# Kernel tuning notes

Measured on AMD Instinct MI355X. Metric: run time of the kernel, lower is better.

## Reference

```python
import jax, jax.numpy as jnp
import numpy as np

N_NODES = 10000
N_EDGES = 160000
MUL0 = 128   # multiplicity of 0e in node input/output
MUL1 = 64    # multiplicity of 1o in node input/output
FC_IN = 8    # radial basis size (edge_scalar_attr dim)
FC_H = 64    # fc_neurons = [64, 64]
NUM_NEIGHBORS = 16.0
ANGLE = np.pi / 8.0
MID0 = MUL0 + MUL1   # 192 scalars in irreps_mid (simplified)
MID1 = MUL0 + MUL1   # 192 vectors (1o) in irreps_mid


def _inv_sqrt(d):
    return 1.0 / np.sqrt(d)


def setup_inputs() -> dict:
    key = jax.random.key(0)
    ks = jax.random.split(key, 18)
    rn = lambda k, shape: jax.random.normal(k, shape, dtype=jnp.float32)
    inp = {
        'node_input': rn(ks[0], (N_NODES, MUL0 + 3 * MUL1)),
        'edge_attr': rn(ks[1], (N_EDGES, 4)),            # 1x0e + 1x1o spherical harmonics
        'edge_scalar_attr': rn(ks[2], (N_EDGES, FC_IN)),
        # first Linear: node_input -> (node_features || node_self_out)
        'Wa0': rn(ks[3], (MUL0, MUL0)),   # 0e -> 0e (message branch)
        'Wa1': rn(ks[4], (MUL1, MUL1)),   # 1o -> 1o (message branch)
        'Wb0': rn(ks[5], (MUL0, MUL0)),   # 0e -> 0e (self branch)
        'Wb1': rn(ks[6], (MUL1, MUL1)),   # 1o -> 1o (self branch)
        # radial MLP
        'M1': rn(ks[7], (FC_IN, FC_H)),
        'M2': rn(ks[8], (FC_H, FC_H)),
        # per-instruction TP weight generators: [FC_H, mul] ('uvu', v=1 squeezed)
        'Wtp0': rn(ks[9], (FC_H, MUL0)),   # 0e x 0e -> 0e
        'Wtp1': rn(ks[10], (FC_H, MUL0)),  # 0e x 1o -> 1o
        'Wtp2': rn(ks[11], (FC_H, MUL1)),  # 1o x 0e -> 1o
        'Wtp3': rn(ks[12], (FC_H, MUL1)),  # 1o x 1o -> 0e
        # output Linear: irreps_mid (192x0e + 192x1o) -> 128x0e + 64x1o
        'Wo0': rn(ks[13], (MID0, MUL0)),
        'Wo1': rn(ks[14], (MID1, MUL1)),
        'edge_src': jax.random.randint(ks[15], (N_EDGES,), 0, N_NODES),
        'edge_dst': jax.random.randint(ks[16], (N_EDGES,), 0, N_NODES),
    }
    return inp


def _forward(node_input, edge_attr, edge_scalar_attr,
             Wa0, Wa1, Wb0, Wb1, M1, M2,
             Wtp0, Wtp1, Wtp2, Wtp3, Wo0, Wo1,
             edge_src, edge_dst):
    n = node_input.shape[0]
    x0 = node_input[:, :MUL0]                         # [N,128] 0e
    x1 = node_input[:, MUL0:].reshape(n, MUL1, 3)     # [N,64,3] 1o

    # Linear(node_input.irreps + irreps_node_output): split into message / self
    feat0 = (x0 @ Wa0) * _inv_sqrt(MUL0)
    feat1 = jnp.einsum('nvi,vu->nui', x1, Wa1) * _inv_sqrt(MUL1)
    self0 = (x0 @ Wb0) * _inv_sqrt(MUL0)
    self1 = jnp.einsum('nvi,vu->nui', x1, Wb1) * _inv_sqrt(MUL1)

    # gather node features to edges
    e0 = feat0[edge_src]                              # [E,128]
    e1 = feat1[edge_src]                              # [E,64,3]
    y0 = edge_attr[:, 0:1]                            # [E,1] 0e
    y1 = edge_attr[:, 1:4]                            # [E,3] 1o

    # radial MLP -> per-edge per-path 'uvu' weights (path param / sqrt(fc_out))
    h = jax.nn.gelu(edge_scalar_attr @ M1 * _inv_sqrt(FC_IN))
    h = jax.nn.gelu(h @ M2 * _inv_sqrt(FC_H))
    w0 = h @ Wtp0 * _inv_sqrt(FC_H)                   # [E,128]
    w1 = h @ Wtp1 * _inv_sqrt(FC_H)                   # [E,128]
    w2 = h @ Wtp2 * _inv_sqrt(FC_H)                   # [E,64]
    w3 = h @ Wtp3 * _inv_sqrt(FC_H)                   # [E,64]

    # CG tensor product paths (component normalization: alpha = sqrt(dim_out))
    mid0a = w0 * e0 * y0                                        # 0e x 0e -> 0e [E,128]
    mid0b = w3 * jnp.einsum('eui,ei->eu', e1, y1) * _inv_sqrt(3.0)  # 1o.1o -> 0e [E,64]
    mid1a = w1[:, :, None] * e0[:, :, None] * y1[:, None, :]   # 0e x 1o -> 1o [E,128,3]
    mid1b = w2[:, :, None] * e1 * y0[:, :, None]                # 1o x 0e -> 1o [E,64,3]

    e_cnt = edge_attr.shape[0]
    edge_mid = jnp.concatenate(
        [mid0a, mid0b, mid1a.reshape(e_cnt, -1), mid1b.reshape(e_cnt, -1)], axis=1)  # [E,768]

    # scatter-add to destination nodes, divide by sqrt(num_neighbors)
    agg = jax.ops.segment_sum(edge_mid, edge_dst, num_segments=n) * _inv_sqrt(NUM_NEIGHBORS)

    z0 = agg[:, :MID0]                                          # [N,192] 0e
    z1 = jnp.concatenate(
        [agg[:, MID0:MID0 + 3 * MUL0].reshape(n, MUL0, 3),
         agg[:, MID0 + 3 * MUL0:].reshape(n, MUL1, 3)], axis=1)  # [N,192,3] 1o

    conv0 = (z0 @ Wo0) * _inv_sqrt(MID0)
    conv1 = jnp.einsum('nvi,vu->nui', z1, Wo1) * _inv_sqrt(MID1)

    c = np.cos(ANGLE).astype(np.float32)
    s = np.sin(ANGLE).astype(np.float32)
    out0 = c * self0 + s * conv0                                 # [N,128]
    out1 = c * self1 + s * conv1                                 # [N,64,3]
    return jnp.concatenate([out0, out1.reshape(n, -1)], axis=1)  # [N,320]


def reference(node_input, edge_attr, edge_scalar_attr,
              Wa0, Wa1, Wb0, Wb1, M1, M2,
              Wtp0, Wtp1, Wtp2, Wtp3, Wo0, Wo1,
              edge_src, edge_dst):
    return _forward(node_input, edge_attr, edge_scalar_attr,
                    Wa0, Wa1, Wb0, Wb1, M1, M2,
                    Wtp0, Wtp1, Wtp2, Wtp3, Wo0, Wo1,
                    edge_src, edge_dst)
```

## Files before the change

kernel.cpp:

```cpp
#include <hip/hip_runtime.h>
#include <hip/hip_bf16.h>
#include <hip/hip_fp16.h>

#define N_NODES 10000
#define N_EDGES 160000
#define FEAT_W 320
#define CHUNK 32

typedef _Float16 half8 __attribute__((ext_vector_type(8)));
typedef float f32x4 __attribute__((ext_vector_type(4)));

__device__ __forceinline__ float gelu_tanh(float x) {
    float x3 = x * x * x;
    float y = 0.7978845608028654f * (x + 0.044715f * x3);
    float th = 1.f - 2.f / (__expf(2.f * y) + 1.f);
    return 0.5f * x * (1.f + th);
}

__global__ __launch_bounds__(320) void prep_kernel(
    const float* __restrict__ node_input,
    const float* __restrict__ Wa0, const float* __restrict__ Wa1,
    const float* __restrict__ Wb0, const float* __restrict__ Wb1,
    float* __restrict__ feat_tbl, float* __restrict__ self_tbl,
    const int* __restrict__ edge_dst, int* __restrict__ counts,
    int* __restrict__ rank,
    const float* __restrict__ Wtp0, const float* __restrict__ Wtp1,
    const float* __restrict__ Wtp2, const float* __restrict__ Wtp3,
    const float* __restrict__ Wo0,  const float* __restrict__ Wo1,
    __half* __restrict__ wtp_pack, __half* __restrict__ wo_pack)
{
    __shared__ __align__(16) float xT[FEAT_W][8];
    const int t = threadIdx.x;

    if (blockIdx.x < 1250) {
        const int node0 = blockIdx.x * 8;
        for (int q = t; q < 640; q += 320) {
            const int n = q / 80, c4 = q - n * 80;
            const float4 v = ((const float4*)(node_input + (size_t)(node0 + n) * FEAT_W))[c4];
            xT[c4 * 4 + 0][n] = v.x; xT[c4 * 4 + 1][n] = v.y;
            xT[c4 * 4 + 2][n] = v.z; xT[c4 * 4 + 3][n] = v.w;
        }
        __syncthreads();

        float accf[8] = {0,0,0,0,0,0,0,0}, accs[8] = {0,0,0,0,0,0,0,0};
        float scale;
        if (t < 128) {
            for (int v = 0; v < 128; ++v) {
                const float wa = Wa0[v * 128 + t];
                const float wb = Wb0[v * 128 + t];
                const float4 xa = *(const float4*)&xT[v][0];
                const float4 xb = *(const float4*)&xT[v][4];
                accf[0] += xa.x * wa; accf[1] += xa.y * wa; accf[2] += xa.z * wa; accf[3] += xa.w * wa;
                accf[4] += xb.x * wa; accf[5] += xb.y * wa; accf[6] += xb.z * wa; accf[7] += xb.w * wa;
                accs[0] += xa.x * wb; accs[1] += xa.y * wb; accs[2] += xa.z * wb; accs[3] += xa.w * wb;
                accs[4] += xb.x * wb; accs[5] += xb.y * wb; accs[6] += xb.z * wb; accs[7] += xb.w * wb;
            }
            scale = 0.08838834764831845f;
        } else {
            const int r = t - 128, u = r / 3, i = r - 3 * u;
            for (int v = 0; v < 64; ++v) {
                const float wa = Wa1[v * 64 + u];
                const float wb = Wb1[v * 64 + u];
                const int row = 128 + v * 3 + i;
                const float4 xa = *(const float4*)&xT[row][0];
                const float4 xb = *(const float4*)&xT[row][4];
                accf[0] += xa.x * wa; accf[1] += xa.y * wa; accf[2] += xa.z * wa; accf[3] += xa.w * wa;
                accf[4] += xb.x * wa; accf[5] += xb.y * wa; accf[6] += xb.z * wa; accf[7] += xb.w * wa;
                accs[0] += xa.x * wb; accs[1] += xa.y * wb; accs[2] += xa.z * wb; accs[3] += xa.w * wb;
                accs[4] += xb.x * wb; accs[5] += xb.y * wb; accs[6] += xb.z * wb; accs[7] += xb.w * wb;
            }
            scale = 0.125f;
        }
#pragma unroll
        for (int n = 0; n < 8; ++n) {
            feat_tbl[(size_t)(node0 + n) * FEAT_W + t] = accf[n] * scale;
            self_tbl[(size_t)(node0 + n) * FEAT_W + t] = accs[n] * scale;
        }
    } else if (blockIdx.x < 1750) {
        const int e = (blockIdx.x - 1250) * 320 + t;
        rank[e] = atomicAdd(&counts[edge_dst[e]], 1);
    } else {
        const int gid = (blockIdx.x - 1750) * 320 + t;
        if (gid < 1536) {
            const int lane = gid & 63;
            const int tile = gid >> 6;
            const int quad = lane >> 4, n16 = lane & 15;
            const int col = tile * 16 + n16;
            const float* src; int stride;
            if (col < 128)      { src = Wtp0 + col;         stride = 128; }
            else if (col < 256) { src = Wtp1 + (col - 128); stride = 128; }
            else if (col < 320) { src = Wtp2 + (col - 256); stride = 64;  }
            else                { src = Wtp3 + (col - 320); stride = 64;  }
            __half* dst = wtp_pack + (size_t)gid * 16;
#pragma unroll
            for (int s = 0; s < 2; ++s)
#pragma unroll
                for (int j = 0; j < 8; ++j)
                    dst[s * 8 + j] = (__half)src[(s * 32 + quad * 8 + j) * stride];
        } else if (gid < 38400) {
            const int i = gid - 1536;
            if (i < 24576) wo_pack[i] = (__half)Wo0[i];
            else           wo_pack[i] = (__half)Wo1[i - 24576];
        }
    }
}

__global__ __launch_bounds__(1024) void scan_kernel(
    const int* __restrict__ counts, int* __restrict__ offsets)
{
    __shared__ int wsum[16];
    const int wid = threadIdx.x >> 6, lane = threadIdx.x & 63;
    int base = 0;
    for (int c = 0; c < 10; ++c) {
        const int i = c * 1024 + threadIdx.x;
        const int v = (i < N_NODES) ? counts[i] : 0;
        int x = v;
#pragma unroll
        for (int off = 1; off < 64; off <<= 1) {
            int y = __shfl_up(x, off, 64);
            if (lane >= off) x += y;
        }
        if (lane == 63) wsum[wid] = x;
        __syncthreads();
        if (threadIdx.x < 16) {
            int s = wsum[threadIdx.x];
#pragma unroll
            for (int off = 1; off < 16; off <<= 1) {
                int y = __shfl_up(s, off, 64);
                if ((int)threadIdx.x >= off) s += y;
            }
            wsum[threadIdx.x] = s;
        }
        __syncthreads();
        const int waveoff = (wid == 0) ? 0 : wsum[wid - 1];
        const int excl = base + waveoff + x - v;
        if (i < N_NODES) offsets[i] = excl;
        const int tot = wsum[15];
        __syncthreads();
        base += tot;
    }
    if (threadIdx.x == 0) offsets[N_NODES] = base;
}

__global__ __launch_bounds__(256) void mlp_kernel(
    const float* __restrict__ esa,
    const float* __restrict__ M1,
    const float* __restrict__ M2,
    const int* __restrict__ edge_dst,
    const int* __restrict__ rank,
    const int* __restrict__ offsets,
    const int* __restrict__ edge_src,
    const float* __restrict__ edge_attr,
    __half* __restrict__ h2csr,
    int* __restrict__ srcs_csr,
    float* __restrict__ y4csr)
{
    __shared__ __align__(16) float sh[4][8][64];
    const int wave = threadIdx.x >> 6;
    const int lane = threadIdx.x & 63;
    const int e0 = blockIdx.x * 32 + wave * 8;

    int pos_l = 0;
    if (lane < 8) {
        const int e = e0 + lane;
        pos_l = offsets[edge_dst[e]] + rank[e];
        srcs_csr[pos_l] = edge_src[e];
        ((float4*)y4csr)[pos_l] = ((const float4*)edge_attr)[e];
    }

    const float mye = esa[(size_t)e0 * 8 + lane];

    float m1k[8];
#pragma unroll
    for (int k = 0; k < 8; ++k) m1k[k] = M1[k * 64 + lane];

#pragma unroll
    for (int g = 0; g < 8; ++g) {
        float h = 0.f;
#pragma unroll
        for (int k = 0; k < 8; ++k)
            h += __shfl(mye, g * 8 + k, 64) * m1k[k];
        sh[wave][g][lane] = gelu_tanh(h * 0.35355339059327373f);
    }
    __syncthreads();

    float h2[8] = {0,0,0,0,0,0,0,0};
#pragma unroll 4
    for (int q = 0; q < 16; ++q) {
        const float m0 = M2[(4 * q + 0) * 64 + lane];
        const float m1_ = M2[(4 * q + 1) * 64 + lane];
        const float m2_ = M2[(4 * q + 2) * 64 + lane];
        const float m3 = M2[(4 * q + 3) * 64 + lane];
#pragma unroll
        for (int g = 0; g < 8; ++g) {
            const float4 s = *(const float4*)&sh[wave][g][q * 4];
            h2[g] += s.x * m0 + s.y * m1_ + s.z * m2_ + s.w * m3;
        }
    }
#pragma unroll
    for (int g = 0; g < 8; ++g) {
        const float v = gelu_tanh(h2[g] * 0.125f) * 0.125f;
        const int pg = __shfl(pos_l, g, 64);
        h2csr[(size_t)pg * 64 + lane] = (__half)v;
    }
}

__global__ __launch_bounds__(384, 4) void gather_kernel(
    const int* __restrict__ offsets,
    const int* __restrict__ srcs_csr,
    const float* __restrict__ y4csr,
    const __half* __restrict__ h2csr,
    const __half* __restrict__ wtp_pack,
    const float* __restrict__ feat_tbl,
    const float* __restrict__ self_tbl,
    const __half* __restrict__ wo_pack,
    float* __restrict__ out)
{
    __shared__ __align__(16) __half wsh[CHUNK * 384];
    __shared__ __align__(16) char pool[CHUNK * 128];
    __shared__ float ys[CHUNK][4];
    __shared__ int   srcs[CHUNK];
    __half* h2s = (__half*)pool;
    float*  z   = (float*)pool;

    const int node = blockIdx.x;
    const int t = threadIdx.x;
    const int wave = t >> 6, lane = t & 63;
    const int quad = lane >> 4, n16 = lane & 15;

    const int beg = offsets[node], end = offsets[node + 1];

    int cb = beg;
    int ne = min(CHUNK, end - cb);
    half8 hreg = {};
    int   sreg = 0;
    float4 yreg = {0.f, 0.f, 0.f, 0.f};
    if (t < ne * 8) hreg = ((const half8*)(h2csr + (size_t)cb * 64))[t];
    if (t < ne)     { sreg = srcs_csr[cb + t]; yreg = ((const float4*)y4csr)[cb + t]; }

    half8 bf[4][2];
#pragma unroll
    for (int c = 0; c < 4; ++c) {
        const __half* p = wtp_pack + (size_t)((wave * 4 + c) * 64 + lane) * 16;
        bf[c][0] = *(const half8*)p;
        bf[c][1] = *(const half8*)(p + 8);
    }

    int f0;
    if (t < 128)      f0 = t;
    else if (t < 256) f0 = t - 128;
    else if (t < 320) f0 = 128 + 3 * (t - 256);
    else              f0 = 128 + 3 * (t - 320);

    float acc = 0.f, acc3a = 0.f, acc3b = 0.f, acc3c = 0.f;

    for (;;) {
        if (t < ne) { srcs[t] = sreg; ((float4*)ys)[t] = yreg; }
        if (t < ne * 8) {
            const int eL = t >> 3, u = t & 7;
            *(half8*)((char*)h2s + eL * 128 + ((u * 16) ^ ((eL & 7) << 4))) = hreg;
        }
        __syncthreads();

#pragma unroll
        for (int g = 0; g < 2; ++g) {
            if (g * 16 < ne) {
                const int e = g * 16 + n16;
                const char* hb = (const char*)h2s + e * 128;
                const int sw = (e & 7) << 4;
                const half8 af0 = *(const half8*)(hb + ((quad * 16) ^ sw));
                const half8 af1 = *(const half8*)(hb + ((64 + quad * 16) ^ sw));
#pragma unroll
                for (int c = 0; c < 4; ++c) {
                    f32x4 acc4 = {0.f, 0.f, 0.f, 0.f};
                    acc4 = __builtin_amdgcn_mfma_f32_16x16x32_f16(af0, bf[c][0], acc4, 0, 0, 0);
                    acc4 = __builtin_amdgcn_mfma_f32_16x16x32_f16(af1, bf[c][1], acc4, 0, 0, 0);
                    const int colb = ((wave * 4 + c) * 16 + n16) * 2;
#pragma unroll
                    for (int r = 0; r < 4; ++r) {
                        const int row = g * 16 + quad * 4 + r;
                        *(__half*)((char*)wsh + row * 768 + (colb ^ (quad << 5))) =
                            (__half)acc4[r];
                    }
                }
            }
        }

        const int cb2 = cb + CHUNK;
        const int ne2 = (cb2 < end) ? min(CHUNK, end - cb2) : 0;
        if (t < ne2 * 8) hreg = ((const half8*)(h2csr + (size_t)cb2 * 64))[t];
        if (t < ne2)     { sreg = srcs_csr[cb2 + t]; yreg = ((const float4*)y4csr)[cb2 + t]; }
        __syncthreads();

        const int tb = t * 2;
#define WRD(ee) __half2float(*(const __half*)((const char*)wsh + (ee) * 768 + (tb ^ ((((ee) >> 2) & 3) << 5))))
        if (t < 128) {
            int e = 0;
            for (; e + 4 <= ne; e += 4) {
                float w4[4], v4[4]; int s4[4];
#pragma unroll
                for (int k = 0; k < 4; ++k) { w4[k] = WRD(e + k); s4[k] = srcs[e + k]; }
#pragma unroll
                for (int k = 0; k < 4; ++k) v4[k] = feat_tbl[(size_t)s4[k] * FEAT_W + f0];
#pragma unroll
                for (int k = 0; k < 4; ++k) acc += w4[k] * v4[k] * ys[e + k][0];
            }
            for (; e < ne; ++e)
                acc += WRD(e) * feat_tbl[(size_t)srcs[e] * FEAT_W + f0] * ys[e][0];
        } else if (t < 256) {
            int e = 0;
            for (; e + 4 <= ne; e += 4) {
                float w4[4], v4[4]; int s4[4];
#pragma unroll
                for (int k = 0; k < 4; ++k) { w4[k] = WRD(e + k); s4[k] = srcs[e + k]; }
#pragma unroll
                for (int k = 0; k < 4; ++k) v4[k] = feat_tbl[(size_t)s4[k] * FEAT_W + f0];
#pragma unroll
                for (int k = 0; k < 4; ++k) {
                    const float p = w4[k] * v4[k];
                    acc3a += p * ys[e + k][1];
                    acc3b += p * ys[e + k][2];
                    acc3c += p * ys[e + k][3];
                }
            }
            for (; e < ne; ++e) {
                const float p = WRD(e) * feat_tbl[(size_t)srcs[e] * FEAT_W + f0];
                acc3a += p * ys[e][1]; acc3b += p * ys[e][2]; acc3c += p * ys[e][3];
            }
        } else if (t < 320) {
            int e = 0;
            for (; e + 4 <= ne; e += 4) {
                float w4[4], va[4], vb[4], vc[4]; int s4[4];
#pragma unroll
                for (int k = 0; k < 4; ++k) { w4[k] = WRD(e + k); s4[k] = srcs[e + k]; }
#pragma unroll
                for (int k = 0; k < 4; ++k) {
                    const float* fr = feat_tbl + (size_t)s4[k] * FEAT_W;
                    va[k] = fr[f0]; vb[k] = fr[f0 + 1]; vc[k] = fr[f0 + 2];
                }
#pragma unroll
                for (int k = 0; k < 4; ++k) {
                    const float p = w4[k] * ys[e + k][0];
                    acc3a += p * va[k]; acc3b += p * vb[k]; acc3c += p * vc[k];
                }
            }
            for (; e < ne; ++e) {
                const float* fr = feat_tbl + (size_t)srcs[e] * FEAT_W;
                const float p = WRD(e) * ys[e][0];
                acc3a += p * fr[f0]; acc3b += p * fr[f0 + 1]; acc3c += p * fr[f0 + 2];
            }
        } else {
            int e = 0;
            for (; e + 4 <= ne; e += 4) {
                float w4[4], va[4], vb[4], vc[4]; int s4[4];
#pragma unroll
                for (int k = 0; k < 4; ++k) { w4[k] = WRD(e + k); s4[k] = srcs[e + k]; }
#pragma unroll
                for (int k = 0; k < 4; ++k) {
                    const float* fr = feat_tbl + (size_t)s4[k] * FEAT_W;
                    va[k] = fr[f0]; vb[k] = fr[f0 + 1]; vc[k] = fr[f0 + 2];
                }
#pragma unroll
                for (int k = 0; k < 4; ++k)
                    acc += w4[k] * (va[k] * ys[e + k][1] + vb[k] * ys[e + k][2]
                                  + vc[k] * ys[e + k][3]);
            }
            for (; e < ne; ++e) {
                const float* fr = feat_tbl + (size_t)srcs[e] * FEAT_W;
                acc += WRD(e) * (fr[f0] * ys[e][1] + fr[f0 + 1] * ys[e][2]
                               + fr[f0 + 2] * ys[e][3]);
            }
        }
#undef WRD

        if (!ne2) break;
        cb = cb2; ne = ne2;
        __syncthreads();
    }

    const float sZ = 0.25f;
    if (t < 128) {
        z[t] = acc * sZ;
    } else if (t < 256) {
        const int u = t - 128;
        z[192 + 0 * 192 + u] = acc3a * sZ;
        z[192 + 1 * 192 + u] = acc3b * sZ;
        z[192 + 2 * 192 + u] = acc3c * sZ;
    } else if (t < 320) {
        const int u = t - 256;
        z[192 + 0 * 192 + 128 + u] = acc3a * sZ;
        z[192 + 1 * 192 + 128 + u] = acc3b * sZ;
        z[192 + 2 * 192 + 128 + u] = acc3c * sZ;
    } else {
        z[128 + (t - 320)] = acc * sZ * 0.5773502691896258f;
    }
    __syncthreads();

    const float sA = 0.07216878364870323f;
    const float cR = 0.92387953251128674f;
    const float sR = 0.38268343236508978f;
    const __half* Wo0h = wo_pack;
    const __half* Wo1h = wo_pack + 24576;

    if (t < 128) {
        float conv = 0.f;
        const float4* z4 = (const float4*)z;
#pragma unroll 8
        for (int q = 0; q < 48; ++q) {
            const float4 zz = z4[q];
            conv += zz.x * (float)Wo0h[(4 * q + 0) * 128 + t];
            conv += zz.y * (float)Wo0h[(4 * q + 1) * 128 + t];
            conv += zz.z * (float)Wo0h[(4 * q + 2) * 128 + t];
            conv += zz.w * (float)Wo0h[(4 * q + 3) * 128 + t];
        }
        const float sv = self_tbl[(size_t)node * FEAT_W + t];
        out[(size_t)node * FEAT_W + t] = cR * sv + sR * conv * sA;
    } else if (t < 320) {
        const int idx = t - 128;
        const int i = idx >> 6, u = idx & 63;
        float conv = 0.f;
        const float4* z4 = (const float4*)(z + 192 + i * 192);
#pragma unroll 8
        for (int q = 0; q < 48; ++q) {
            const float4 zz = z4[q];
            conv += zz.x * (float)Wo1h[(4 * q + 0) * 64 + u];
            conv += zz.y * (float)Wo1h[(4 * q + 1) * 64 + u];
            conv += zz.z * (float)Wo1h[(4 * q + 2) * 64 + u];
            conv += zz.w * (float)Wo1h[(4 * q + 3) * 64 + u];
        }
        const int col = 128 + u * 3 + i;
        const float sv = self_tbl[(size_t)node * FEAT_W + col];
        out[(size_t)node * FEAT_W + col] = cR * sv + sR * conv * sA;
    }
}

extern "C" void kernel_launch(void* const* d_in, const int* in_sizes, int n_in,
                              void* d_out, int out_size, void* d_ws, size_t ws_size,
                              hipStream_t stream) {
    const float* node_input = (const float*)d_in[0];
    const float* edge_attr  = (const float*)d_in[1];
    const float* esa        = (const float*)d_in[2];
    const float* Wa0  = (const float*)d_in[3];
    const float* Wa1  = (const float*)d_in[4];
    const float* Wb0  = (const float*)d_in[5];
    const float* Wb1  = (const float*)d_in[6];
    const float* M1   = (const float*)d_in[7];
    const float* M2   = (const float*)d_in[8];
    const float* Wtp0 = (const float*)d_in[9];
    const float* Wtp1 = (const float*)d_in[10];
    const float* Wtp2 = (const float*)d_in[11];
    const float* Wtp3 = (const float*)d_in[12];
    const float* Wo0  = (const float*)d_in[13];
    const float* Wo1  = (const float*)d_in[14];
    const int* edge_src = (const int*)d_in[15];
    const int* edge_dst = (const int*)d_in[16];
    float* out = (float*)d_out;

    char* w = (char*)d_ws;
    float*  feat_tbl = (float*)w;           w += (size_t)N_NODES * FEAT_W * 4;
    float*  self_tbl = (float*)w;           w += (size_t)N_NODES * FEAT_W * 4;
    float*  y4csr    = (float*)w;           w += (size_t)N_EDGES * 4 * 4;
    __half* h2csr    = (__half*)w;          w += (size_t)N_EDGES * 64 * 2;
    __half* wtp_pack = (__half*)w;          w += (size_t)24576 * 2;
    __half* wo_pack  = (__half*)w;          w += (size_t)36864 * 2;
    int*    counts   = (int*)w;             w += (size_t)N_NODES * 4;
    int*    offsets  = (int*)w;             w += (size_t)(N_NODES + 1) * 4;
    int*    rank     = (int*)w;             w += (size_t)N_EDGES * 4;
    int*    srcs_csr = (int*)w;             w += (size_t)N_EDGES * 4;

    hipMemsetAsync(counts, 0, sizeof(int) * N_NODES, stream);

    prep_kernel<<<1870, 320, 0, stream>>>(node_input, Wa0, Wa1, Wb0, Wb1,
                                          feat_tbl, self_tbl,
                                          edge_dst, counts, rank,
                                          Wtp0, Wtp1, Wtp2, Wtp3, Wo0, Wo1,
                                          wtp_pack, wo_pack);
    scan_kernel<<<1, 1024, 0, stream>>>(counts, offsets);
    mlp_kernel<<<N_EDGES / 32, 256, 0, stream>>>(esa, M1, M2, edge_dst, rank, offsets,
                                                 edge_src, edge_attr,
                                                 h2csr, srcs_csr, y4csr);
    gather_kernel<<<N_NODES, 384, 0, stream>>>(offsets, srcs_csr, y4csr, h2csr,
                                               wtp_pack, feat_tbl, self_tbl,
                                               wo_pack, out);
}
```

Baseline: 331.0 us.

## Stage gathered source feature rows in LDS with vectorized loads, halve chunk size

Each chunk's source-node feature rows are now copied cooperatively into shared memory with coalesced float4 loads. The per-thread accumulation loops then read from LDS instead of issuing scattered scalar global loads, which were duplicated across thread groups and strided by three for the vector part. CHUNK drops from 32 to 16 so the extra 20KB staging buffer fits, and the MFMA weight-generation step is cut to a single 16-row tile. The cost is more chunk iterations and barriers for high-degree nodes, plus higher LDS use per block, which may limit occupancy.

```diff
diff --git a/kernel.cpp b/kernel.cpp
--- a/kernel.cpp
+++ b/kernel.cpp
@@ -5,7 +5,7 @@
 #define N_NODES 10000
 #define N_EDGES 160000
 #define FEAT_W 320
-#define CHUNK 32
+#define CHUNK 16
 
 typedef _Float16 half8 __attribute__((ext_vector_type(8)));
 typedef float f32x4 __attribute__((ext_vector_type(4)));
@@ -217,7 +217,8 @@
     float* __restrict__ out)
 {
     __shared__ __align__(16) __half wsh[CHUNK * 384];
-    __shared__ __align__(16) char pool[CHUNK * 128];
+    __shared__ __align__(16) float fsh[CHUNK * FEAT_W];
+    __shared__ __align__(16) char pool[4096];
     __shared__ float ys[CHUNK][4];
     __shared__ int   srcs[CHUNK];
     __half* h2s = (__half*)pool;
@@ -262,26 +263,29 @@
         }
         __syncthreads();
 
-#pragma unroll
-        for (int g = 0; g < 2; ++g) {
-            if (g * 16 < ne) {
-                const int e = g * 16 + n16;
-                const char* hb = (const char*)h2s + e * 128;
-                const int sw = (e & 7) << 4;
-                const half8 af0 = *(const half8*)(hb + ((quad * 16) ^ sw));
-                const half8 af1 = *(const half8*)(hb + ((64 + quad * 16) ^ sw));
-#pragma unroll
-                for (int c = 0; c < 4; ++c) {
-                    f32x4 acc4 = {0.f, 0.f, 0.f, 0.f};
-                    acc4 = __builtin_amdgcn_mfma_f32_16x16x32_f16(af0, bf[c][0], acc4, 0, 0, 0);
-                    acc4 = __builtin_amdgcn_mfma_f32_16x16x32_f16(af1, bf[c][1], acc4, 0, 0, 0);
-                    const int colb = ((wave * 4 + c) * 16 + n16) * 2;
-#pragma unroll
-                    for (int r = 0; r < 4; ++r) {
-                        const int row = g * 16 + quad * 4 + r;
-                        *(__half*)((char*)wsh + row * 768 + (colb ^ (quad << 5))) =
-                            (__half)acc4[r];
-                    }
+        for (int q = t; q < ne * 80; q += 384) {
+            const int eL = q / 80, c4 = q - eL * 80;
+            ((float4*)fsh)[eL * 80 + c4] =
+                ((const float4*)(feat_tbl + (size_t)srcs[eL] * FEAT_W))[c4];
+        }
+
+        if (ne > 0) {
+            const int e = n16;
+            const char* hb = (const char*)h2s + e * 128;
+            const int sw = (e & 7) << 4;
+            const half8 af0 = *(const half8*)(hb + ((quad * 16) ^ sw));
+            const half8 af1 = *(const half8*)(hb + ((64 + quad * 16) ^ sw));
+#pragma unroll
+            for (int c = 0; c < 4; ++c) {
+                f32x4 acc4 = {0.f, 0.f, 0.f, 0.f};
+                acc4 = __builtin_amdgcn_mfma_f32_16x16x32_f16(af0, bf[c][0], acc4, 0, 0, 0);
+                acc4 = __builtin_amdgcn_mfma_f32_16x16x32_f16(af1, bf[c][1], acc4, 0, 0, 0);
+                const int colb = ((wave * 4 + c) * 16 + n16) * 2;
+#pragma unroll
+                for (int r = 0; r < 4; ++r) {
+                    const int row = quad * 4 + r;
+                    *(__half*)((char*)wsh + row * 768 + (colb ^ (quad << 5))) =
+                        (__half)acc4[r];
                 }
             }
         }
@@ -297,24 +301,20 @@
         if (t < 128) {
             int e = 0;
             for (; e + 4 <= ne; e += 4) {
-                float w4[4], v4[4]; int s4[4];
-#pragma unroll
-                for (int k = 0; k < 4; ++k) { w4[k] = WRD(e + k); s4[k] = srcs[e + k]; }
-#pragma unroll
-                for (int k = 0; k < 4; ++k) v4[k] = feat_tbl[(size_t)s4[k] * FEAT_W + f0];
+                float w4[4], v4[4];
+#pragma unroll
+                for (int k = 0; k < 4; ++k) { w4[k] = WRD(e + k); v4[k] = fsh[(e + k) * FEAT_W + f0]; }
 #pragma unroll
                 for (int k = 0; k < 4; ++k) acc += w4[k] * v4[k] * ys[e + k][0];
             }
             for (; e < ne; ++e)
-                acc += WRD(e) * feat_tbl[(size_t)srcs[e] * FEAT_W + f0] * ys[e][0];
+                acc += WRD(e) * fsh[e * FEAT_W + f0] * ys[e][0];
         } else if (t < 256) {
             int e = 0;
             for (; e + 4 <= ne; e += 4) {
-                float w4[4], v4[4]; int s4[4];
-#pragma unroll
-                for (int k = 0; k < 4; ++k) { w4[k] = WRD(e + k); s4[k] = srcs[e + k]; }
-#pragma unroll
-                for (int k = 0; k < 4; ++k) v4[k] = feat_tbl[(size_t)s4[k] * FEAT_W + f0];
+                float w4[4], v4[4];
+#pragma unroll
+                for (int k = 0; k < 4; ++k) { w4[k] = WRD(e + k); v4[k] = fsh[(e + k) * FEAT_W + f0]; }
 #pragma unroll
                 for (int k = 0; k < 4; ++k) {
                     const float p = w4[k] * v4[k];
@@ -324,18 +324,17 @@
                 }
             }
             for (; e < ne; ++e) {
-                const float p = WRD(e) * feat_tbl[(size_t)srcs[e] * FEAT_W + f0];
+                const float p = WRD(e) * fsh[e * FEAT_W + f0];
                 acc3a += p * ys[e][1]; acc3b += p * ys[e][2]; acc3c += p * ys[e][3];
             }
         } else if (t < 320) {
             int e = 0;
             for (; e + 4 <= ne; e += 4) {
-                float w4[4], va[4], vb[4], vc[4]; int s4[4];
-#pragma unroll
-                for (int k = 0; k < 4; ++k) { w4[k] = WRD(e + k); s4[k] = srcs[e + k]; }
+                float w4[4], va[4], vb[4], vc[4];
 #pragma unroll
                 for (int k = 0; k < 4; ++k) {
-                    const float* fr = feat_tbl + (size_t)s4[k] * FEAT_W;
+                    w4[k] = WRD(e + k);
+                    const float* fr = fsh + (e + k) * FEAT_W;
                     va[k] = fr[f0]; vb[k] = fr[f0 + 1]; vc[k] = fr[f0 + 2];
                 }
 #pragma unroll
@@ -345,19 +344,18 @@
                 }
             }
             for (; e < ne; ++e) {
-                const float* fr = feat_tbl + (size_t)srcs[e] * FEAT_W;
+                const float* fr = fsh + e * FEAT_W;
                 const float p = WRD(e) * ys[e][0];
                 acc3a += p * fr[f0]; acc3b += p * fr[f0 + 1]; acc3c += p * fr[f0 + 2];
             }
         } else {
             int e = 0;
             for (; e + 4 <= ne; e += 4) {
-                float w4[4], va[4], vb[4], vc[4]; int s4[4];
-#pragma unroll
-                for (int k = 0; k < 4; ++k) { w4[k] = WRD(e + k); s4[k] = srcs[e + k]; }
+                float w4[4], va[4], vb[4], vc[4];
 #pragma unroll
                 for (int k = 0; k < 4; ++k) {
-                    const float* fr = feat_tbl + (size_t)s4[k] * FEAT_W;
+                    w4[k] = WRD(e + k);
+                    const float* fr = fsh + (e + k) * FEAT_W;
                     va[k] = fr[f0]; vb[k] = fr[f0 + 1]; vc[k] = fr[f0 + 2];
                 }
 #pragma unroll
@@ -366,7 +364,7 @@
                                   + vc[k] * ys[e + k][3]);
             }
             for (; e < ne; ++e) {
-                const float* fr = feat_tbl + (size_t)srcs[e] * FEAT_W;
+                const float* fr = fsh + e * FEAT_W;
                 acc += WRD(e) * (fr[f0] * ys[e][1] + fr[f0 + 1] * ys[e][2]
                                + fr[f0 + 2] * ys[e][3]);
             }
```

New measurement: 355.4 us. 7.4% more time.

## Move radial MLP into prep kernel, gather h2 via edge list indirection

Applied to the files above, without the earlier changes.

The radial MLP now runs as extra blocks inside the prep kernel, before the scan, and writes h2 in original edge order. A light fill kernel builds the CSR arrays plus an edge-index list. The gather kernel then fetches h2 rows indirectly through that list. The aim is to take the MLP off the critical path after the scan and overlap it with the node linear work, at the cost of non-contiguous h2 reads in the gather.

```diff
diff --git a/kernel.cpp b/kernel.cpp
--- a/kernel.cpp
+++ b/kernel.cpp
@@ -27,12 +27,15 @@
     const float* __restrict__ Wtp0, const float* __restrict__ Wtp1,
     const float* __restrict__ Wtp2, const float* __restrict__ Wtp3,
     const float* __restrict__ Wo0,  const float* __restrict__ Wo1,
-    __half* __restrict__ wtp_pack, __half* __restrict__ wo_pack)
+    __half* __restrict__ wtp_pack, __half* __restrict__ wo_pack,
+    const float* __restrict__ esa, const float* __restrict__ M1,
+    const float* __restrict__ M2,  __half* __restrict__ h2edge)
 {
-    __shared__ __align__(16) float xT[FEAT_W][8];
+    __shared__ __align__(16) float shm[FEAT_W * 8];
     const int t = threadIdx.x;
 
     if (blockIdx.x < 1250) {
+        float (*xT)[8] = (float(*)[8])shm;
         const int node0 = blockIdx.x * 8;
         for (int q = t; q < 640; q += 320) {
             const int n = q / 80, c4 = q - n * 80;
@@ -79,7 +82,7 @@
     } else if (blockIdx.x < 1750) {
         const int e = (blockIdx.x - 1250) * 320 + t;
         rank[e] = atomicAdd(&counts[edge_dst[e]], 1);
-    } else {
+    } else if (blockIdx.x < 1870) {
         const int gid = (blockIdx.x - 1750) * 320 + t;
         if (gid < 1536) {
             const int lane = gid & 63;
@@ -102,6 +105,46 @@
             if (i < 24576) wo_pack[i] = (__half)Wo0[i];
             else           wo_pack[i] = (__half)Wo1[i - 24576];
         }
+    } else {
+        float (*sh)[64] = (float(*)[64])shm;
+        const int wave = t >> 6;
+        const int lane = t & 63;
+        const int e0 = (blockIdx.x - 1870) * 40 + wave * 8;
+
+        const float mye = esa[(size_t)e0 * 8 + lane];
+
+        float m1k[8];
+#pragma unroll
+        for (int k = 0; k < 8; ++k) m1k[k] = M1[k * 64 + lane];
+
+#pragma unroll
+        for (int g = 0; g < 8; ++g) {
+            float h = 0.f;
+#pragma unroll
+            for (int k = 0; k < 8; ++k)
+                h += __shfl(mye, g * 8 + k, 64) * m1k[k];
+            sh[wave * 8 + g][lane] = gelu_tanh(h * 0.35355339059327373f);
+        }
+        __syncthreads();
+
+        float h2[8] = {0,0,0,0,0,0,0,0};
+#pragma unroll 4
+        for (int q = 0; q < 16; ++q) {
+            const float m0 = M2[(4 * q + 0) * 64 + lane];
+            const float m1_ = M2[(4 * q + 1) * 64 + lane];
+            const float m2_ = M2[(4 * q + 2) * 64 + lane];
+            const float m3 = M2[(4 * q + 3) * 64 + lane];
+#pragma unroll
+            for (int g = 0; g < 8; ++g) {
+                const float4 s = *(const float4*)&sh[wave * 8 + g][q * 4];
+                h2[g] += s.x * m0 + s.y * m1_ + s.z * m2_ + s.w * m3;
+            }
+        }
+#pragma unroll
+        for (int g = 0; g < 8; ++g) {
+            const float v = gelu_tanh(h2[g] * 0.125f) * 0.125f;
+            h2edge[(size_t)(e0 + g) * 64 + lane] = (__half)v;
+        }
     }
 }
 
@@ -142,74 +185,26 @@
     if (threadIdx.x == 0) offsets[N_NODES] = base;
 }
 
-__global__ __launch_bounds__(256) void mlp_kernel(
-    const float* __restrict__ esa,
-    const float* __restrict__ M1,
-    const float* __restrict__ M2,
-    const int* __restrict__ edge_dst,
-    const int* __restrict__ rank,
-    const int* __restrict__ offsets,
-    const int* __restrict__ edge_src,
+__global__ __launch_bounds__(256) void fill_kernel(
+    const int* __restrict__ edge_dst, const int* __restrict__ rank,
+    const int* __restrict__ offsets,  const int* __restrict__ edge_src,
     const float* __restrict__ edge_attr,
-    __half* __restrict__ h2csr,
-    int* __restrict__ srcs_csr,
+    int* __restrict__ elist, int* __restrict__ srcs_csr,
     float* __restrict__ y4csr)
 {
-    __shared__ __align__(16) float sh[4][8][64];
-    const int wave = threadIdx.x >> 6;
-    const int lane = threadIdx.x & 63;
-    const int e0 = blockIdx.x * 32 + wave * 8;
-
-    int pos_l = 0;
-    if (lane < 8) {
-        const int e = e0 + lane;
-        pos_l = offsets[edge_dst[e]] + rank[e];
-        srcs_csr[pos_l] = edge_src[e];
-        ((float4*)y4csr)[pos_l] = ((const float4*)edge_attr)[e];
-    }
-
-    const float mye = esa[(size_t)e0 * 8 + lane];
-
-    float m1k[8];
-#pragma unroll
-    for (int k = 0; k < 8; ++k) m1k[k] = M1[k * 64 + lane];
-
-#pragma unroll
-    for (int g = 0; g < 8; ++g) {
-        float h = 0.f;
-#pragma unroll
-        for (int k = 0; k < 8; ++k)
-            h += __shfl(mye, g * 8 + k, 64) * m1k[k];
-        sh[wave][g][lane] = gelu_tanh(h * 0.35355339059327373f);
-    }
-    __syncthreads();
-
-    float h2[8] = {0,0,0,0,0,0,0,0};
-#pragma unroll 4
-    for (int q = 0; q < 16; ++q) {
-        const float m0 = M2[(4 * q + 0) * 64 + lane];
-        const float m1_ = M2[(4 * q + 1) * 64 + lane];
-        const float m2_ = M2[(4 * q + 2) * 64 + lane];
-        const float m3 = M2[(4 * q + 3) * 64 + lane];
-#pragma unroll
-        for (int g = 0; g < 8; ++g) {
-            const float4 s = *(const float4*)&sh[wave][g][q * 4];
-            h2[g] += s.x * m0 + s.y * m1_ + s.z * m2_ + s.w * m3;
-        }
-    }
-#pragma unroll
-    for (int g = 0; g < 8; ++g) {
-        const float v = gelu_tanh(h2[g] * 0.125f) * 0.125f;
-        const int pg = __shfl(pos_l, g, 64);
-        h2csr[(size_t)pg * 64 + lane] = (__half)v;
-    }
+    const int e = blockIdx.x * 256 + threadIdx.x;
+    const int pos = offsets[edge_dst[e]] + rank[e];
+    elist[pos] = e;
+    srcs_csr[pos] = edge_src[e];
+    ((float4*)y4csr)[pos] = ((const float4*)edge_attr)[e];
 }
 
 __global__ __launch_bounds__(384, 4) void gather_kernel(
     const int* __restrict__ offsets,
+    const int* __restrict__ elist,
     const int* __restrict__ srcs_csr,
     const float* __restrict__ y4csr,
-    const __half* __restrict__ h2csr,
+    const __half* __restrict__ h2edge,
     const __half* __restrict__ wtp_pack,
     const float* __restrict__ feat_tbl,
     const float* __restrict__ self_tbl,
@@ -235,7 +230,10 @@
     half8 hreg = {};
     int   sreg = 0;
     float4 yreg = {0.f, 0.f, 0.f, 0.f};
-    if (t < ne * 8) hreg = ((const half8*)(h2csr + (size_t)cb * 64))[t];
+    if (t < ne * 8) {
+        const int el = elist[cb + (t >> 3)];
+        hreg = ((const half8*)(h2edge + (size_t)el * 64))[t & 7];
+    }
     if (t < ne)     { sreg = srcs_csr[cb + t]; yreg = ((const float4*)y4csr)[cb + t]; }
 
     half8 bf[4][2];
@@ -288,7 +286,10 @@
 
         const int cb2 = cb + CHUNK;
         const int ne2 = (cb2 < end) ? min(CHUNK, end - cb2) : 0;
-        if (t < ne2 * 8) hreg = ((const half8*)(h2csr + (size_t)cb2 * 64))[t];
+        if (t < ne2 * 8) {
+            const int el = elist[cb2 + (t >> 3)];
+            hreg = ((const half8*)(h2edge + (size_t)el * 64))[t & 7];
+        }
         if (t < ne2)     { sreg = srcs_csr[cb2 + t]; yreg = ((const float4*)y4csr)[cb2 + t]; }
         __syncthreads();
 
@@ -460,26 +461,28 @@
     float*  feat_tbl = (float*)w;           w += (size_t)N_NODES * FEAT_W * 4;
     float*  self_tbl = (float*)w;           w += (size_t)N_NODES * FEAT_W * 4;
     float*  y4csr    = (float*)w;           w += (size_t)N_EDGES * 4 * 4;
-    __half* h2csr    = (__half*)w;          w += (size_t)N_EDGES * 64 * 2;
+    __half* h2edge   = (__half*)w;          w += (size_t)N_EDGES * 64 * 2;
     __half* wtp_pack = (__half*)w;          w += (size_t)24576 * 2;
     __half* wo_pack  = (__half*)w;          w += (size_t)36864 * 2;
     int*    counts   = (int*)w;             w += (size_t)N_NODES * 4;
     int*    offsets  = (int*)w;             w += (size_t)(N_NODES + 1) * 4;
     int*    rank     = (int*)w;             w += (size_t)N_EDGES * 4;
     int*    srcs_csr = (int*)w;             w += (size_t)N_EDGES * 4;
+    int*    elist    = (int*)w;             w += (size_t)N_EDGES * 4;
 
     hipMemsetAsync(counts, 0, sizeof(int) * N_NODES, stream);
 
-    prep_kernel<<<1870, 320, 0, stream>>>(node_input, Wa0, Wa1, Wb0, Wb1,
+    prep_kernel<<<5870, 320, 0, stream>>>(node_input, Wa0, Wa1, Wb0, Wb1,
                                           feat_tbl, self_tbl,
                                           edge_dst, counts, rank,
                                           Wtp0, Wtp1, Wtp2, Wtp3, Wo0, Wo1,
-                                          wtp_pack, wo_pack);
+                                          wtp_pack, wo_pack,
+                                          esa, M1, M2, h2edge);
     scan_kernel<<<1, 1024, 0, stream>>>(counts, offsets);
-    mlp_kernel<<<N_EDGES / 32, 256, 0, stream>>>(esa, M1, M2, edge_dst, rank, offsets,
-                                                 edge_src, edge_attr,
-                                                 h2csr, srcs_csr, y4csr);
-    gather_kernel<<<N_NODES, 384, 0, stream>>>(offsets, srcs_csr, y4csr, h2csr,
-                                               wtp_pack, feat_tbl, self_tbl,
-                                               wo_pack, out);
-}
+    fill_kernel<<<N_EDGES / 256, 256, 0, stream>>>(edge_dst, rank, offsets,
+                                                   edge_src, edge_attr,
+                                                   elist, srcs_csr, y4csr);
+    gather_kernel<<<N_NODES, 384, 0, stream>>>(offsets, elist, srcs_csr, y4csr,
+                                               h2edge, wtp_pack, feat_tbl,
+                                               self_tbl, wo_pack, out);
+}
```

New measurement: 411.1 us. 1.24x slower.
